# Kernel tuning notes

Measured on AMD Instinct MI355X. Metric: run time of the kernel, lower is better.

The kernel has to match this reference:

```python
import jax, jax.numpy as jnp
import numpy as np

N_NODES = 50000
EMBED_DIM = 100
N_RAND_EDGES = 600000
NEG_SLOPE = 0.2  # alpha in the original module


def _build_pairs(n_nodes, n_edges, seed=0):
    """Replicates: neighbors(v) = unique(out_nbrs(v) U in_nbrs(v)) for all v,
    flattened into (seg=v, nbr=u) pair arrays (symmetrized, deduped edge list)."""
    rng = np.random.default_rng(seed)
    src = rng.integers(0, n_nodes, n_edges)
    dst = rng.integers(0, n_nodes, n_edges)
    ring = np.arange(n_nodes)  # guarantee every node has a neighbor
    src = np.concatenate([src, ring])
    dst = np.concatenate([dst, (ring + 1) % n_nodes])
    seg = np.concatenate([src, dst])
    nbr = np.concatenate([dst, src])
    pairs = np.unique(np.stack([seg, nbr], axis=1), axis=0)  # sorted by seg
    return pairs[:, 0].astype(np.int32), pairs[:, 1].astype(np.int32)


def setup_inputs() -> dict:
    key = jax.random.key(0)
    k1, k2 = jax.random.split(key)
    hidden = jax.random.normal(k1, (N_NODES, EMBED_DIM), dtype=jnp.float32)
    # nn.Linear(embed_dim, 1, bias=False) weight, kaiming-uniform-ish scale
    W = jax.random.normal(k2, (EMBED_DIM,), dtype=jnp.float32) / np.sqrt(EMBED_DIM)
    seg_np, nbr_np = _build_pairs(N_NODES, N_RAND_EDGES)
    return {"hidden": hidden, "W": W,
            "seg": jnp.asarray(seg_np), "nbr": jnp.asarray(nbr_np)}


def reference(hidden, W, seg, nbr):
    n = hidden.shape[0]
    h_i = hidden[seg]            # [P, D] center node repeated per neighbor
    h_j = hidden[nbr]            # [P, D] gathered neighbor embeddings
    scores = jnp.einsum('pd,d->p', h_i * h_j, W)           # a(neighbors*hidden)
    scores = jnp.where(scores >= 0, scores, NEG_SLOPE * scores)  # leaky_relu
    # per-node (segment) softmax, numerically stable
    m = jax.ops.segment_max(scores, seg, num_segments=n)
    e = jnp.exp(scores - m[seg])
    z = jax.ops.segment_sum(e, seg, num_segments=n)
    alpha = e / z[seg]                                      # [P]
    out = jax.ops.segment_sum(alpha[:, None] * h_j, seg, num_segments=n)  # [N, D]
    return out
```

## Files before the change

### kernel.cpp

```cpp
#include <hip/hip_runtime.h>
#include <math.h>

#define D 100
#define NEG_SLOPE 0.2f
#define CHUNK 16
#define ROWU 52

#define COMPILER_FENCE() asm volatile("" ::: "memory")

typedef _Float16 f16x2 __attribute__((ext_vector_type(2)));
union U32H2 { unsigned int u; f16x2 h; };

__device__ __forceinline__ unsigned int pkh2(float x, float y) {
    U32H2 c; c.h.x = (_Float16)x; c.h.y = (_Float16)y; return c.u;
}

__device__ __forceinline__ float dot2u(unsigned int au, unsigned int xu, float acc) {
#if __has_builtin(__builtin_amdgcn_fdot2)
    U32H2 a, x; a.u = au; x.u = xu;
    return __builtin_amdgcn_fdot2(a.h, x.h, acc, false);
#else
    U32H2 a, x; a.u = au; x.u = xu;
    return acc + (float)a.h.x * (float)x.h.x + (float)a.h.y * (float)x.h.y;
#endif
}

template<int CTRL>
__device__ __forceinline__ float dppf(float x) {
    return __uint_as_float((unsigned)__builtin_amdgcn_update_dpp(
        0, (int)__float_as_uint(x), CTRL, 0xF, 0xF, true));
}
__device__ __forceinline__ float red16_max(float x) {
    x = fmaxf(x, dppf<0xB1>(x));
    x = fmaxf(x, dppf<0x4E>(x));
    x = fmaxf(x, dppf<0x124>(x));
    x = fmaxf(x, dppf<0x128>(x));
    return x;
}
__device__ __forceinline__ float red16_sum(float x) {
    x += dppf<0xB1>(x);
    x += dppf<0x4E>(x);
    x += dppf<0x124>(x);
    x += dppf<0x128>(x);
    return x;
}

__global__ void prep_kernel(const int* __restrict__ seg,
                            int* __restrict__ row_ptr,
                            const float* __restrict__ hidden,
                            unsigned int* __restrict__ hb,
                            int n, int P, int total25)
{
    int t = blockIdx.x * blockDim.x + threadIdx.x;
    if (t < P) {
        int s0 = seg[t];
        if (t == 0)
            for (int v = 0; v <= s0; v++) row_ptr[v] = 0;
        int s1 = (t + 1 < P) ? seg[t + 1] : n;
        for (int v = s0 + 1; v <= s1; v++) row_ptr[v] = t + 1;
    }
    if (t < total25) {
        int node = t / 25, k = t - node * 25;
        float4 f = ((const float4*)hidden)[t];
        *(uint2*)&hb[node * ROWU + 2 * k] =
            make_uint2(pkh2(f.x, f.y), pkh2(f.z, f.w));
    }
}

__launch_bounds__(256, 8)
__global__ void gat_agg_kernel(const float* __restrict__ hidden,
                               const float* __restrict__ W,
                               const int* __restrict__ nbr,
                               const int* __restrict__ row_ptr,
                               const unsigned int* __restrict__ hb,
                               float* __restrict__ out,
                               int n, int P)
{
    __shared__ __align__(16) unsigned int s_hwp[4][ROWU];
    __shared__ __align__(16) unsigned int s_rows[4][CHUNK][ROWU];
    __shared__ __align__(16) float        s_e[4][CHUNK];

    const int lane = threadIdx.x & 63;
    const int wid  = threadIdx.x >> 6;
    const int v    = blockIdx.x * 4 + wid;
    if (v >= n) return;

    if (lane < 50) {
        float2 h2 = ((const float2*)(hidden + (long)v * D))[lane];
        float2 w2 = ((const float2*)W)[lane];
        s_hwp[wid][lane] = pkh2(h2.x * w2.x, h2.y * w2.y);
    }
    COMPILER_FENCE();

    const int start = row_ptr[v];
    const int end   = row_ptr[v + 1];

    if (end <= start) {
        if (lane < D / 2)
            ((float2*)(out + (long)v * D))[lane] = make_float2(0.f, 0.f);
        return;
    }

    const int preN = nbr[min(start + lane, P - 1)];

    const int q  = lane >> 4;
    const int jl = lane & 15;
    const int t0 = q * 3;

    const uint4* hwq = ((const uint4*)&s_hwp[wid][0]) + t0;
    const uint4 a0 = hwq[0], a1 = hwq[1], a2 = hwq[2];
    uint2 at = make_uint2(0u, 0u);
    if (q == 0) at = *(const uint2*)&s_hwp[wid][48];

    float m = -INFINITY, z = 0.f;
    float accx = 0.f, accy = 0.f;

    for (int c = start; c < end; c += CHUNK) {
        const int  cnt = min(CHUNK, end - c);
        const bool pv  = jl < cnt;
        const int  off = c - start;

        int nbv;
        if (off + CHUNK <= 64) {
            nbv = __shfl(preN, off + jl, 64);
            nbv = pv ? nbv : 0;
        } else {
            nbv = pv ? nbr[c + jl] : 0;
        }
        const uint4* row16 = ((const uint4*)hb) + nbv * (ROWU / 4) + t0;

        uint4 x0 = row16[0], x1 = row16[1], x2 = row16[2];
        uint2 xt = make_uint2(0u, 0u);
        if (q == 0) xt = *(const uint2*)&hb[nbv * ROWU + 48];

        float p0 = 0.f, p1 = 0.f, p2 = 0.f, p3 = 0.f;
        p0 = dot2u(a0.x, x0.x, p0);  p1 = dot2u(a0.y, x0.y, p1);
        p2 = dot2u(a0.z, x0.z, p2);  p3 = dot2u(a0.w, x0.w, p3);
        p0 = dot2u(a1.x, x1.x, p0);  p1 = dot2u(a1.y, x1.y, p1);
        p2 = dot2u(a1.z, x1.z, p2);  p3 = dot2u(a1.w, x1.w, p3);
        p0 = dot2u(a2.x, x2.x, p0);  p1 = dot2u(a2.y, x2.y, p1);
        p2 = dot2u(a2.z, x2.z, p2);  p3 = dot2u(a2.w, x2.w, p3);
        if (q == 0) {
            p0 = dot2u(at.x, xt.x, p0);
            p1 = dot2u(at.y, xt.y, p1);
        }

        uint4* dst16 = ((uint4*)&s_rows[wid][jl][0]) + t0;
        dst16[0] = x0; dst16[1] = x1; dst16[2] = x2;
        if (q == 0) *(uint2*)&s_rows[wid][jl][48] = xt;

        float part = (p0 + p1) + (p2 + p3);
        part += __shfl_xor(part, 16, 64);
        part += __shfl_xor(part, 32, 64);
        const float s = pv ? (part >= 0.f ? part : NEG_SLOPE * part)
                           : -INFINITY;

        const float m_new = fmaxf(m, red16_max(s));
        const float scale = __expf(m - m_new);
        const float e     = pv ? __expf(s - m_new) : 0.f;
        z = z * scale + red16_sum(e);
        accx *= scale; accy *= scale;

        if (lane < CHUNK) s_e[wid][lane] = e;
        COMPILER_FENCE();

        const int cnt4 = (cnt + 3) & ~3;
        if (lane < D / 2) {
            for (int j0 = 0; j0 < cnt4; j0 += 4) {
                const float4 ev = *(const float4*)&s_e[wid][j0];
                U32H2 u0, u1, u2, u3;
                u0.u = s_rows[wid][j0    ][lane];
                u1.u = s_rows[wid][j0 + 1][lane];
                u2.u = s_rows[wid][j0 + 2][lane];
                u3.u = s_rows[wid][j0 + 3][lane];
                accx = fmaf((float)u0.h.x, ev.x, accx);
                accy = fmaf((float)u0.h.y, ev.x, accy);
                accx = fmaf((float)u1.h.x, ev.y, accx);
                accy = fmaf((float)u1.h.y, ev.y, accy);
                accx = fmaf((float)u2.h.x, ev.z, accx);
                accy = fmaf((float)u2.h.y, ev.z, accy);
                accx = fmaf((float)u3.h.x, ev.w, accx);
                accy = fmaf((float)u3.h.y, ev.w, accy);
            }
        }
        COMPILER_FENCE();
        m = m_new;
    }

    if (lane < D / 2) {
        const float inv = 1.f / z;
        ((float2*)(out + (long)v * D))[lane] = make_float2(accx * inv, accy * inv);
    }
}

extern "C" void kernel_launch(void* const* d_in, const int* in_sizes, int n_in,
                              void* d_out, int out_size, void* d_ws, size_t ws_size,
                              hipStream_t stream) {
    const float* hidden = (const float*)d_in[0];
    const float* W      = (const float*)d_in[1];
    const int*   seg    = (const int*)d_in[2];
    const int*   nbr    = (const int*)d_in[3];
    float*       out    = (float*)d_out;

    const int Ddim = in_sizes[1];
    const int n    = in_sizes[0] / Ddim;
    const int P    = in_sizes[2];

    int* row_ptr = (int*)d_ws;
    size_t hb_off = (((size_t)(n + 1) * 4) + 255) & ~(size_t)255;
    unsigned int* hb = (unsigned int*)((char*)d_ws + hb_off);

    const int total25 = n * 25;
    const int tmax    = (P > total25) ? P : total25;
    hipLaunchKernelGGL(prep_kernel, dim3((tmax + 255) / 256), dim3(256), 0, stream,
                       seg, row_ptr, hidden, hb, n, P, total25);
    hipLaunchKernelGGL(gat_agg_kernel, dim3((n + 3) / 4), dim3(256), 0, stream,
                       hidden, W, nbr, row_ptr, hb, out, n, P);
}
```

Measured before the change: 126.4 us.

## Process 32 neighbors per chunk with two lanes per neighbor row

The chunk of neighbors handled per wavefront iteration doubles to 32. The lane mapping changes so each neighbor row is split across two lanes that each load six or seven 16-byte vectors. The fp16 rows and the h*W vector are zero-padded to 52 entries so the split needs no tail special case, and the shuffled prefetch of neighbor indices is replaced by direct loads. With an average degree around 26, most nodes should now finish in one iteration instead of two, at the cost of more registers and longer serial loads per lane.

```diff
diff --git a/kernel.cpp b/kernel.cpp
--- a/kernel.cpp
+++ b/kernel.cpp
@@ -3,7 +3,7 @@
 
 #define D 100
 #define NEG_SLOPE 0.2f
-#define CHUNK 16
+#define CHUNK 32
 #define ROWU 52
 
 #define COMPILER_FENCE() asm volatile("" ::: "memory")
@@ -65,6 +65,9 @@
         *(uint2*)&hb[node * ROWU + 2 * k] =
             make_uint2(pkh2(f.x, f.y), pkh2(f.z, f.w));
     }
+    if (t < n) {
+        *(uint2*)&hb[(size_t)t * ROWU + 50] = make_uint2(0u, 0u);
+    }
 }
 
 __launch_bounds__(256, 8)
@@ -85,10 +88,14 @@
     const int v    = blockIdx.x * 4 + wid;
     if (v >= n) return;
 
-    if (lane < 50) {
-        float2 h2 = ((const float2*)(hidden + (long)v * D))[lane];
-        float2 w2 = ((const float2*)W)[lane];
-        s_hwp[wid][lane] = pkh2(h2.x * w2.x, h2.y * w2.y);
+    if (lane < ROWU) {
+        unsigned int val = 0u;
+        if (lane < 50) {
+            float2 h2 = ((const float2*)(hidden + (long)v * D))[lane];
+            float2 w2 = ((const float2*)W)[lane];
+            val = pkh2(h2.x * w2.x, h2.y * w2.y);
+        }
+        s_hwp[wid][lane] = val;
     }
     COMPILER_FENCE();
 
@@ -101,16 +108,11 @@
         return;
     }
 
-    const int preN = nbr[min(start + lane, P - 1)];
-
-    const int q  = lane >> 4;
-    const int jl = lane & 15;
-    const int t0 = q * 3;
-
-    const uint4* hwq = ((const uint4*)&s_hwp[wid][0]) + t0;
-    const uint4 a0 = hwq[0], a1 = hwq[1], a2 = hwq[2];
-    uint2 at = make_uint2(0u, 0u);
-    if (q == 0) at = *(const uint2*)&s_hwp[wid][48];
+    const int q  = lane >> 5;
+    const int jl = lane & 31;
+    const int t0 = q * 7;
+
+    const uint4* aq = ((const uint4*)&s_hwp[wid][0]) + t0;
 
     float m = -INFINITY, z = 0.f;
     float accx = 0.f, accy = 0.f;
@@ -118,47 +120,52 @@
     for (int c = start; c < end; c += CHUNK) {
         const int  cnt = min(CHUNK, end - c);
         const bool pv  = jl < cnt;
-        const int  off = c - start;
-
-        int nbv;
-        if (off + CHUNK <= 64) {
-            nbv = __shfl(preN, off + jl, 64);
-            nbv = pv ? nbv : 0;
-        } else {
-            nbv = pv ? nbr[c + jl] : 0;
+
+        const int nbv = pv ? nbr[c + jl] : 0;
+
+        const uint4* rp = ((const uint4*)hb) + nbv * (ROWU / 4) + t0;
+        uint4 x0 = rp[0], x1 = rp[1], x2 = rp[2],
+              x3 = rp[3], x4 = rp[4], x5 = rp[5];
+        uint4 x6 = make_uint4(0u, 0u, 0u, 0u);
+        if (q == 0) x6 = rp[6];
+
+        uint4* dst = ((uint4*)&s_rows[wid][jl][0]) + t0;
+        dst[0] = x0; dst[1] = x1; dst[2] = x2;
+        dst[3] = x3; dst[4] = x4; dst[5] = x5;
+        if (q == 0) dst[6] = x6;
+
+        float p0 = 0.f, p1 = 0.f, p2 = 0.f, p3 = 0.f;
+        uint4 a;
+        a = aq[0]; p0 = dot2u(a.x, x0.x, p0); p1 = dot2u(a.y, x0.y, p1);
+                   p2 = dot2u(a.z, x0.z, p2); p3 = dot2u(a.w, x0.w, p3);
+        a = aq[1]; p0 = dot2u(a.x, x1.x, p0); p1 = dot2u(a.y, x1.y, p1);
+                   p2 = dot2u(a.z, x1.z, p2); p3 = dot2u(a.w, x1.w, p3);
+        a = aq[2]; p0 = dot2u(a.x, x2.x, p0); p1 = dot2u(a.y, x2.y, p1);
+                   p2 = dot2u(a.z, x2.z, p2); p3 = dot2u(a.w, x2.w, p3);
+        a = aq[3]; p0 = dot2u(a.x, x3.x, p0); p1 = dot2u(a.y, x3.y, p1);
+                   p2 = dot2u(a.z, x3.z, p2); p3 = dot2u(a.w, x3.w, p3);
+        a = aq[4]; p0 = dot2u(a.x, x4.x, p0); p1 = dot2u(a.y, x4.y, p1);
+                   p2 = dot2u(a.z, x4.z, p2); p3 = dot2u(a.w, x4.w, p3);
+        a = aq[5]; p0 = dot2u(a.x, x5.x, p0); p1 = dot2u(a.y, x5.y, p1);
+                   p2 = dot2u(a.z, x5.z, p2); p3 = dot2u(a.w, x5.w, p3);
+        if (q == 0) {
+            a = aq[6]; p0 = dot2u(a.x, x6.x, p0); p1 = dot2u(a.y, x6.y, p1);
+                       p2 = dot2u(a.z, x6.z, p2); p3 = dot2u(a.w, x6.w, p3);
         }
-        const uint4* row16 = ((const uint4*)hb) + nbv * (ROWU / 4) + t0;
-
-        uint4 x0 = row16[0], x1 = row16[1], x2 = row16[2];
-        uint2 xt = make_uint2(0u, 0u);
-        if (q == 0) xt = *(const uint2*)&hb[nbv * ROWU + 48];
-
-        float p0 = 0.f, p1 = 0.f, p2 = 0.f, p3 = 0.f;
-        p0 = dot2u(a0.x, x0.x, p0);  p1 = dot2u(a0.y, x0.y, p1);
-        p2 = dot2u(a0.z, x0.z, p2);  p3 = dot2u(a0.w, x0.w, p3);
-        p0 = dot2u(a1.x, x1.x, p0);  p1 = dot2u(a1.y, x1.y, p1);
-        p2 = dot2u(a1.z, x1.z, p2);  p3 = dot2u(a1.w, x1.w, p3);
-        p0 = dot2u(a2.x, x2.x, p0);  p1 = dot2u(a2.y, x2.y, p1);
-        p2 = dot2u(a2.z, x2.z, p2);  p3 = dot2u(a2.w, x2.w, p3);
-        if (q == 0) {
-            p0 = dot2u(at.x, xt.x, p0);
-            p1 = dot2u(at.y, xt.y, p1);
-        }
-
-        uint4* dst16 = ((uint4*)&s_rows[wid][jl][0]) + t0;
-        dst16[0] = x0; dst16[1] = x1; dst16[2] = x2;
-        if (q == 0) *(uint2*)&s_rows[wid][jl][48] = xt;
 
         float part = (p0 + p1) + (p2 + p3);
-        part += __shfl_xor(part, 16, 64);
         part += __shfl_xor(part, 32, 64);
         const float s = pv ? (part >= 0.f ? part : NEG_SLOPE * part)
                            : -INFINITY;
 
-        const float m_new = fmaxf(m, red16_max(s));
+        float gmax = red16_max(s);
+        gmax = fmaxf(gmax, __shfl_xor(gmax, 16, 64));
+        const float m_new = fmaxf(m, gmax);
         const float scale = __expf(m - m_new);
         const float e     = pv ? __expf(s - m_new) : 0.f;
-        z = z * scale + red16_sum(e);
+        float gsum = red16_sum(e);
+        gsum += __shfl_xor(gsum, 16, 64);
+        z = z * scale + gsum;
         accx *= scale; accy *= scale;
 
         if (lane < CHUNK) s_e[wid][lane] = e;
```

After: 137.7 us. 9.0% more time.
